# Kernel tuning notes

Hardware: AMD Instinct MI355X
Metric: run time of the kernel (lower is better)

Reference implementation:

```python
import jax, jax.numpy as jnp
import numpy as np

BSZ, KDIM, UDIM, T = 2048, 64, 16, 30


def setup_inputs() -> dict:
    key = jax.random.key(0)
    k0, k1, k2, k3, k4 = jax.random.split(key, 5)
    I_k = jnp.eye(KDIM, dtype=jnp.float32)
    I_u = jnp.eye(UDIM, dtype=jnp.float32)
    # Stabilized dynamics (spectral radius ~<1) so the T-step Riccati recursion stays finite.
    A = 0.9 * I_k + 0.02 * jax.random.normal(k0, (BSZ, KDIM, KDIM), dtype=jnp.float32)
    B = 0.1 * jax.random.normal(k1, (BSZ, KDIM, UDIM), dtype=jnp.float32)
    q = 0.1 * jax.random.normal(k2, (BSZ, KDIM, KDIM), dtype=jnp.float32)
    Q = jnp.einsum('bij,bkj->bik', q, q) + I_k  # SPD cost
    r = 0.1 * jax.random.normal(k3, (BSZ, UDIM, UDIM), dtype=jnp.float32)
    R = jnp.einsum('bij,bkj->bik', r, r) + I_u  # SPD control cost
    goals = jax.random.normal(k4, (BSZ, T + 1, KDIM), dtype=jnp.float32)
    return {"A": A, "B": B, "Q": Q, "R": R, "goals": goals}


def reference(A, B, Q, R, goals):
    # Faithful port of KoopmanLQR._solve_lqr: backward Riccati recursion.
    T_h = goals.shape[1] - 1
    AT = jnp.swapaxes(A, -2, -1)
    BT = jnp.swapaxes(B, -2, -1)
    V0 = Q
    v0 = jnp.einsum('bij,bj->bi', Q, goals[:, -1, :])
    # time-major goals for steps T-1 .. 0 (reversed)
    goals_rev = jnp.swapaxes(goals[:, :T_h, :], 0, 1)[::-1]  # [T, B, k]

    def step(carry, goal_i):
        V, v = carry
        Vuu = BT @ V @ B + R                         # [B,u,u]
        Vuu_inv = jnp.linalg.pinv(Vuu)
        Kg = Vuu_inv @ BT @ V @ A                    # [B,u,k] feedback gain
        kg = jnp.einsum('bij,bj->bi', Vuu_inv @ BT, v)  # [B,u] feedforward
        A_BK = A - B @ Kg
        V_new = AT @ V @ A_BK + Q
        v_new = jnp.einsum('bji,bj->bi', A_BK, v) + jnp.einsum('bij,bj->bi', Q, goal_i)
        return (V_new, v_new), (Kg, kg)

    (_, _), (K_rev, k_rev) = jax.lax.scan(step, (V0, v0), goals_rev)
    K_all = K_rev[::-1]  # [T,B,u,k], K_all[i] == K[i] of the torch loop
    k_all = k_rev[::-1]  # [T,B,u]
    # pack gains and feedforward terms in one array: [T,B,u,k+1]
    return jnp.concatenate([K_all, k_all[..., None]], axis=-1)
```

## Files before the change

### kernel.cpp

```cpp
#include <hip/hip_runtime.h>

#define KD 64
#define UD 16
#define TH 30
#define NT 256

typedef short bf16x8 __attribute__((ext_vector_type(8)));
typedef float f32x4 __attribute__((ext_vector_type(4)));
typedef unsigned short u16x4 __attribute__((ext_vector_type(4)));

__device__ __forceinline__ void f2hl(float f, unsigned short& h, unsigned short& l) {
  unsigned int ub = __float_as_uint(f);
  h = (unsigned short)(ub >> 16);
  float fh = __uint_as_float(ub & 0xffff0000u);
  l = (unsigned short)(__float_as_uint(f - fh) >> 16);
}
__device__ __forceinline__ float rec(unsigned short h, unsigned short l) {
  return __uint_as_float((unsigned int)h << 16) + __uint_as_float((unsigned int)l << 16);
}

__device__ __forceinline__ bf16x8 ld64(const unsigned short* buf, int row, int kcg) {
  return *(const bf16x8*)(buf + row * 64 + ((kcg ^ (row & 7)) << 3));
}
__device__ __forceinline__ bf16x8 ld16(const unsigned short* buf, int row, int g) {
  if (g < 2) return *(const bf16x8*)(buf + row * 16 + (g << 3));
  bf16x8 z = {};
  return z;
}
__device__ __forceinline__ void st64_4(unsigned short* buf, int row, int col0, u16x4 v) {
  int off = row * 64 + ((((col0 >> 3)) ^ (row & 7)) << 3) + (col0 & 7);
  *(u16x4*)(buf + off) = v;
}
__device__ __forceinline__ void st16_4(unsigned short* buf, int row, int col0, u16x4 v) {
  *(u16x4*)(buf + row * 16 + col0) = v;
}
__device__ __forceinline__ void cvt4(f32x4 a, u16x4& h, u16x4& l) {
  #pragma unroll
  for (int i = 0; i < 4; ++i) {
    unsigned short hh, ll;
    f2hl(a[i], hh, ll);
    h[i] = hh; l[i] = ll;
  }
}

#define MFMA3(ACC, XH, XL, YH, YL)                                          \
  ACC = __builtin_amdgcn_mfma_f32_16x16x32_bf16(XH, YH, ACC, 0, 0, 0);      \
  ACC = __builtin_amdgcn_mfma_f32_16x16x32_bf16(XH, YL, ACC, 0, 0, 0);      \
  ACC = __builtin_amdgcn_mfma_f32_16x16x32_bf16(XL, YH, ACC, 0, 0, 0);

__global__ __launch_bounds__(NT, 2) void lqr_mfma(
    const float* __restrict__ gA, const float* __restrict__ gB,
    const float* __restrict__ gQ, const float* __restrict__ gR,
    const float* __restrict__ gG, float* __restrict__ gOut, int bsz)
{
  __shared__ unsigned short sVh[64 * 64], sVl[64 * 64];
  __shared__ unsigned short sAth[64 * 64], sAtl[64 * 64];
  __shared__ unsigned short sWth[64 * 64], sWtl[64 * 64];
  __shared__ unsigned short sBth[16 * 64], sBtl[16 * 64];
  __shared__ unsigned short sVBh[16 * 64], sVBl[16 * 64];
  __shared__ unsigned short sBWh[64 * 16], sBWl[64 * 16];
  __shared__ unsigned short sKth[64 * 16], sKtl[64 * 16];
  __shared__ unsigned short sVIh[16 * 16], sVIl[16 * 16];
  __shared__ float sQG[(TH + 1) * 64];
  __shared__ float sVuu[16 * 17];
  __shared__ float sMT[16 * 17];
  __shared__ float sKg[16 * 65];
  __shared__ float sv[64];
  __shared__ float sBtv[16];

  const int b    = blockIdx.x;
  const int tid  = threadIdx.x;
  const int lane = tid & 63;
  const int wv   = tid >> 6;
  const int r    = lane & 15;
  const int g    = lane >> 4;

  const float* Ab = gA + (size_t)b * (64 * 64);
  const float* Bb = gB + (size_t)b * (64 * 16);
  const float* Qb = gQ + (size_t)b * (64 * 64);
  const float* Rb = gR + (size_t)b * (16 * 16);
  const float* Gb = gG + (size_t)b * ((TH + 1) * 64);

  for (int idx = tid; idx < 64 * 64; idx += NT) {
    int k = idx >> 6, i = idx & 63;
    unsigned short h, l;
    f2hl(Ab[idx], h, l);
    int offA = i * 64 + ((((k >> 3)) ^ (i & 7)) << 3) + (k & 7);
    sAth[offA] = h; sAtl[offA] = l;
    f2hl(Qb[idx], h, l);
    int offV = k * 64 + ((((i >> 3)) ^ (k & 7)) << 3) + (i & 7);
    sVh[offV] = h; sVl[offV] = l;
  }
  for (int idx = tid; idx < 64 * 16; idx += NT) {
    int k = idx >> 4, u = idx & 15;
    unsigned short h, l;
    f2hl(Bb[idx], h, l);
    int off = u * 64 + ((((k >> 3)) ^ (u & 7)) << 3) + (k & 7);
    sBth[off] = h; sBtl[off] = l;
  }
  __syncthreads();

  for (int idx = tid; idx < (TH + 1) * 64; idx += NT) {
    int t = idx >> 6, i = idx & 63;
    const float* gt = Gb + t * 64;
    float s = 0.f;
    #pragma unroll 8
    for (int k = 0; k < 64; ++k) {
      int off = i * 64 + ((((k >> 3)) ^ (i & 7)) << 3) + (k & 7);
      s += rec(sVh[off], sVl[off]) * gt[k];
    }
    sQG[idx] = s;
  }
  __syncthreads();
  if (tid < 64) sv[tid] = sQG[TH * 64 + tid];

  f32x4 qreg[4];
  #pragma unroll
  for (int c = 0; c < 4; ++c) {
    #pragma unroll
    for (int rg = 0; rg < 4; ++rg)
      qreg[c][rg] = Qb[(16 * wv + 4 * g + rg) * 64 + 16 * c + r];
  }
  f32x4 rreg;
  #pragma unroll
  for (int rg = 0; rg < 4; ++rg) rreg[rg] = Rb[(4 * g + rg) * 16 + r];

  for (int t = TH - 1; t >= 0; --t) {
    {
      f32x4 accW0 = 0.f, accW1 = 0.f, accW2 = 0.f, accW3 = 0.f, accVB = 0.f;
      #pragma unroll
      for (int kc = 0; kc < 2; ++kc) {
        int kcg = 4 * kc + g;
        bf16x8 xh = ld64(sVh, 16 * wv + r, kcg);
        bf16x8 xl = ld64(sVl, 16 * wv + r, kcg);
        bf16x8 yh, yl;
        yh = ld64(sAth, 0 * 16 + r, kcg); yl = ld64(sAtl, 0 * 16 + r, kcg);
        MFMA3(accW0, xh, xl, yh, yl)
        yh = ld64(sAth, 1 * 16 + r, kcg); yl = ld64(sAtl, 1 * 16 + r, kcg);
        MFMA3(accW1, xh, xl, yh, yl)
        yh = ld64(sAth, 2 * 16 + r, kcg); yl = ld64(sAtl, 2 * 16 + r, kcg);
        MFMA3(accW2, xh, xl, yh, yl)
        yh = ld64(sAth, 3 * 16 + r, kcg); yl = ld64(sAtl, 3 * 16 + r, kcg);
        MFMA3(accW3, xh, xl, yh, yl)
        yh = ld64(sBth, r, kcg); yl = ld64(sBtl, r, kcg);
        MFMA3(accVB, xh, xl, yh, yl)
      }
      u16x4 h4, l4;
      cvt4(accW0, h4, l4); st64_4(sWth, 0 * 16 + r, 16 * wv + 4 * g, h4); st64_4(sWtl, 0 * 16 + r, 16 * wv + 4 * g, l4);
      cvt4(accW1, h4, l4); st64_4(sWth, 1 * 16 + r, 16 * wv + 4 * g, h4); st64_4(sWtl, 1 * 16 + r, 16 * wv + 4 * g, l4);
      cvt4(accW2, h4, l4); st64_4(sWth, 2 * 16 + r, 16 * wv + 4 * g, h4); st64_4(sWtl, 2 * 16 + r, 16 * wv + 4 * g, l4);
      cvt4(accW3, h4, l4); st64_4(sWth, 3 * 16 + r, 16 * wv + 4 * g, h4); st64_4(sWtl, 3 * 16 + r, 16 * wv + 4 * g, l4);
      cvt4(accVB, h4, l4); st64_4(sVBh, r, 16 * wv + 4 * g, h4); st64_4(sVBl, r, 16 * wv + 4 * g, l4);
    }
    __syncthreads();

    if (wv == 0) {
      f32x4 accU = rreg, accBv = 0.f;
      #pragma unroll
      for (int kc = 0; kc < 2; ++kc) {
        int kcg = 4 * kc + g;
        bf16x8 xh = ld64(sBth, r, kcg);
        bf16x8 xl = ld64(sBtl, r, kcg);
        bf16x8 yh = ld64(sVBh, r, kcg);
        bf16x8 yl = ld64(sVBl, r, kcg);
        MFMA3(accU, xh, xl, yh, yl)
        bf16x8 vh = {}, vl = {};
        if (r == 0) {
          #pragma unroll
          for (int e = 0; e < 8; ++e) {
            unsigned short hh, ll;
            f2hl(sv[32 * kc + 8 * g + e], hh, ll);
            vh[e] = (short)hh; vl[e] = (short)ll;
          }
        }
        MFMA3(accBv, xh, xl, vh, vl)
      }
      #pragma unroll
      for (int rg = 0; rg < 4; ++rg) sVuu[(4 * g + rg) * 17 + r] = accU[rg];
      if (r == 0) {
        #pragma unroll
        for (int rg = 0; rg < 4; ++rg) sBtv[4 * g + rg] = accBv[rg];
      }
    } else {
      #pragma unroll
      for (int ci = 0; ci < 2; ++ci) {
        int c = (ci == 0) ? (wv - 1) : ((wv == 1) ? 3 : -1);
        if (c >= 0) {
          f32x4 acc = 0.f;
          #pragma unroll
          for (int kc = 0; kc < 2; ++kc) {
            int kcg = 4 * kc + g;
            bf16x8 xh = ld64(sBth, r, kcg);
            bf16x8 xl = ld64(sBtl, r, kcg);
            bf16x8 yh = ld64(sWth, 16 * c + r, kcg);
            bf16x8 yl = ld64(sWtl, 16 * c + r, kcg);
            MFMA3(acc, xh, xl, yh, yl)
          }
          u16x4 h4, l4; cvt4(acc, h4, l4);
          st16_4(sBWh, 16 * c + r, 4 * g, h4);
          st16_4(sBWl, 16 * c + r, 4 * g, l4);
        }
      }
    }
    __syncthreads();

    if (wv == 0) {
      const int u = lane & 15;
      float rr[16];
      #pragma unroll
      for (int k = 0; k < 16; ++k) rr[k] = sVuu[u * 17 + k];
      #pragma unroll
      for (int j = 0; j < 16; ++j) {
        float s = rr[j];
        #pragma unroll
        for (int k = 0; k < j; ++k) s -= rr[k] * __shfl(rr[k], j);
        const float dj  = sqrtf(__shfl(s, j));
        const float inv = 1.f / dj;
        rr[j] = (u == j) ? dj : s * inv;
      }
      float idia[16];
      #pragma unroll
      for (int i = 0; i < 16; ++i) idia[i] = 1.f / __shfl(rr[i], i);
      float x[16];
      #pragma unroll
      for (int i = 0; i < 16; ++i) {
        float s = (i == u) ? 1.f : 0.f;
        #pragma unroll
        for (int k = 0; k < i; ++k) s -= __shfl(rr[k], i) * x[k];
        x[i] = s * idia[i];
      }
      if (lane < 16) {
        #pragma unroll
        for (int i = 0; i < 16; ++i) sMT[u * 17 + i] = x[i];
      }
    }
    __syncthreads();

    {
      const int a2 = tid & 15, b2 = tid >> 4;
      float s = 0.f;
      #pragma unroll
      for (int i = 0; i < 16; ++i) s += sMT[a2 * 17 + i] * sMT[b2 * 17 + i];
      unsigned short h, l; f2hl(s, h, l);
      sVIh[a2 * 16 + b2] = h; sVIl[a2 * 16 + b2] = l;
    }
    __syncthreads();

    {
      f32x4 acc = 0.f;
      bf16x8 xh = ld16(sVIh, r, g);
      bf16x8 xl = ld16(sVIl, r, g);
      bf16x8 yh = ld16(sBWh, 16 * wv + r, g);
      bf16x8 yl = ld16(sBWl, 16 * wv + r, g);
      MFMA3(acc, xh, xl, yh, yl)
      u16x4 h4, l4;
      f32x4 nacc = -acc;
      cvt4(nacc, h4, l4);
      st16_4(sKth, 16 * wv + r, 4 * g, h4);
      st16_4(sKtl, 16 * wv + r, 4 * g, l4);
      #pragma unroll
      for (int rg = 0; rg < 4; ++rg)
        sKg[(4 * g + rg) * 65 + (16 * wv + r)] = acc[rg];
      if (tid >= 64 && tid < 80) {
        const int uu = tid - 64;
        float s = 0.f;
        #pragma unroll
        for (int w2 = 0; w2 < 16; ++w2)
          s += rec(sVIh[uu * 16 + w2], sVIl[uu * 16 + w2]) * sBtv[w2];
        sKg[uu * 65 + 64] = s;
      }
    }
    __syncthreads();

    {
      const size_t obase = ((size_t)t * bsz + b) * (16 * 65);
      for (int idx = tid; idx < 16 * 65; idx += NT)
        gOut[obase + idx] = sKg[idx];
    }
    if (t > 0) {
      f32x4 acc0 = qreg[0], acc1 = qreg[1], acc2 = qreg[2], acc3 = qreg[3];
      {
        bf16x8 x2h = ld16(sBWh, 16 * wv + r, g);
        bf16x8 x2l = ld16(sBWl, 16 * wv + r, g);
        bf16x8 yh, yl;
        yh = ld16(sKth, 0 * 16 + r, g); yl = ld16(sKtl, 0 * 16 + r, g);
        MFMA3(acc0, x2h, x2l, yh, yl)
        yh = ld16(sKth, 1 * 16 + r, g); yl = ld16(sKtl, 1 * 16 + r, g);
        MFMA3(acc1, x2h, x2l, yh, yl)
        yh = ld16(sKth, 2 * 16 + r, g); yl = ld16(sKtl, 2 * 16 + r, g);
        MFMA3(acc2, x2h, x2l, yh, yl)
        yh = ld16(sKth, 3 * 16 + r, g); yl = ld16(sKtl, 3 * 16 + r, g);
        MFMA3(acc3, x2h, x2l, yh, yl)
      }
      #pragma unroll
      for (int kc = 0; kc < 2; ++kc) {
        int kcg = 4 * kc + g;
        bf16x8 xh = ld64(sAth, 16 * wv + r, kcg);
        bf16x8 xl = ld64(sAtl, 16 * wv + r, kcg);
        bf16x8 yh, yl;
        yh = ld64(sWth, 0 * 16 + r, kcg); yl = ld64(sWtl, 0 * 16 + r, kcg);
        MFMA3(acc0, xh, xl, yh, yl)
        yh = ld64(sWth, 1 * 16 + r, kcg); yl = ld64(sWtl, 1 * 16 + r, kcg);
        MFMA3(acc1, xh, xl, yh, yl)
        yh = ld64(sWth, 2 * 16 + r, kcg); yl = ld64(sWtl, 2 * 16 + r, kcg);
        MFMA3(acc2, xh, xl, yh, yl)
        yh = ld64(sWth, 3 * 16 + r, kcg); yl = ld64(sWtl, 3 * 16 + r, kcg);
        MFMA3(acc3, xh, xl, yh, yl)
      }
      {
        const int i = tid & 63, q = tid >> 6;
        float s = (q == 0) ? sQG[t * 64 + i] : 0.f;
        #pragma unroll
        for (int kk = 0; kk < 16; ++kk) {
          int k = 16 * q + kk;
          int off = i * 64 + ((((k >> 3)) ^ (i & 7)) << 3) + (k & 7);
          s += rec(sAth[off], sAtl[off]) * sv[k];
        }
        #pragma unroll
        for (int uu = 0; uu < 4; ++uu)
          s -= sKg[(4 * q + uu) * 65 + i] * sBtv[4 * q + uu];
        sMT[q * 64 + i] = s;
      }
      u16x4 h4, l4;
      cvt4(acc0, h4, l4); st64_4(sVh, 0 * 16 + r, 16 * wv + 4 * g, h4); st64_4(sVl, 0 * 16 + r, 16 * wv + 4 * g, l4);
      cvt4(acc1, h4, l4); st64_4(sVh, 1 * 16 + r, 16 * wv + 4 * g, h4); st64_4(sVl, 1 * 16 + r, 16 * wv + 4 * g, l4);
      cvt4(acc2, h4, l4); st64_4(sVh, 2 * 16 + r, 16 * wv + 4 * g, h4); st64_4(sVl, 2 * 16 + r, 16 * wv + 4 * g, l4);
      cvt4(acc3, h4, l4); st64_4(sVh, 3 * 16 + r, 16 * wv + 4 * g, h4); st64_4(sVl, 3 * 16 + r, 16 * wv + 4 * g, l4);
      __syncthreads();
      if (tid < 64)
        sv[tid] = sMT[tid] + sMT[64 + tid] + sMT[128 + tid] + sMT[192 + tid];
    }
  }
}

extern "C" void kernel_launch(void* const* d_in, const int* in_sizes, int n_in,
                              void* d_out, int out_size, void* d_ws, size_t ws_size,
                              hipStream_t stream) {
  (void)n_in; (void)out_size; (void)d_ws; (void)ws_size;
  const float* A = (const float*)d_in[0];
  const float* B = (const float*)d_in[1];
  const float* Q = (const float*)d_in[2];
  const float* R = (const float*)d_in[3];
  const float* G = (const float*)d_in[4];
  float* out = (float*)d_out;
  const int bsz = in_sizes[3] / (UD * UD);
  lqr_mfma<<<bsz, NT, 0, stream>>>(A, B, Q, R, G, out, bsz);
}
```

Before: 961.4 us.

## Double block to eight waves and overlap Riccati sub-steps across waves

Moves the kernel from 256 to 512 threads per block and re-partitions each Riccati step so different waves run independent sub-computations at the same time. The A^T·W product overlaps with the Vuu inversion and the B^T·W products, A^T·v moves to MFMA on idle waves, and Q·goals is precomputed with MFMA. The v update is rewritten using B·W and Kg·v instead of a dot with sKg, and gains go straight to global memory without staging through shared memory. BW and K tiles are padded to row stride 24, presumably to reduce bank conflicts. The cost is more waves per block and extra barriers, and the launch bound now targets 4 blocks per CU.

```diff
diff --git a/kernel.cpp b/kernel.cpp
--- a/kernel.cpp
+++ b/kernel.cpp
@@ -1,9 +1,7 @@
 #include <hip/hip_runtime.h>
 
-#define KD 64
-#define UD 16
 #define TH 30
-#define NT 256
+#define NT 512
 
 typedef short bf16x8 __attribute__((ext_vector_type(8)));
 typedef float f32x4 __attribute__((ext_vector_type(4)));
@@ -18,21 +16,24 @@
 __device__ __forceinline__ float rec(unsigned short h, unsigned short l) {
   return __uint_as_float((unsigned int)h << 16) + __uint_as_float((unsigned int)l << 16);
 }
-
 __device__ __forceinline__ bf16x8 ld64(const unsigned short* buf, int row, int kcg) {
   return *(const bf16x8*)(buf + row * 64 + ((kcg ^ (row & 7)) << 3));
 }
-__device__ __forceinline__ bf16x8 ld16(const unsigned short* buf, int row, int g) {
+__device__ __forceinline__ void st64_4(unsigned short* buf, int row, int col0, u16x4 v) {
+  *(u16x4*)(buf + row * 64 + (((col0 >> 3) ^ (row & 7)) << 3) + (col0 & 7)) = v;
+}
+__device__ __forceinline__ bf16x8 ld24(const unsigned short* buf, int row, int g) {
+  if (g < 2) return *(const bf16x8*)(buf + row * 24 + (g << 3));
+  bf16x8 z = {};
+  return z;
+}
+__device__ __forceinline__ void st24_4(unsigned short* buf, int row, int col0, u16x4 v) {
+  *(u16x4*)(buf + row * 24 + col0) = v;
+}
+__device__ __forceinline__ bf16x8 ld16v(const unsigned short* buf, int row, int g) {
   if (g < 2) return *(const bf16x8*)(buf + row * 16 + (g << 3));
   bf16x8 z = {};
   return z;
-}
-__device__ __forceinline__ void st64_4(unsigned short* buf, int row, int col0, u16x4 v) {
-  int off = row * 64 + ((((col0 >> 3)) ^ (row & 7)) << 3) + (col0 & 7);
-  *(u16x4*)(buf + off) = v;
-}
-__device__ __forceinline__ void st16_4(unsigned short* buf, int row, int col0, u16x4 v) {
-  *(u16x4*)(buf + row * 16 + col0) = v;
 }
 __device__ __forceinline__ void cvt4(f32x4 a, u16x4& h, u16x4& l) {
   #pragma unroll
@@ -43,28 +44,29 @@
   }
 }
 
-#define MFMA3(ACC, XH, XL, YH, YL)                                          \
-  ACC = __builtin_amdgcn_mfma_f32_16x16x32_bf16(XH, YH, ACC, 0, 0, 0);      \
-  ACC = __builtin_amdgcn_mfma_f32_16x16x32_bf16(XH, YL, ACC, 0, 0, 0);      \
+#define MFMA3(ACC, XH, XL, YH, YL)                                        \
+  ACC = __builtin_amdgcn_mfma_f32_16x16x32_bf16(XH, YH, ACC, 0, 0, 0);    \
+  ACC = __builtin_amdgcn_mfma_f32_16x16x32_bf16(XH, YL, ACC, 0, 0, 0);    \
   ACC = __builtin_amdgcn_mfma_f32_16x16x32_bf16(XL, YH, ACC, 0, 0, 0);
 
-__global__ __launch_bounds__(NT, 2) void lqr_mfma(
+__global__ __launch_bounds__(NT, 4) void lqr8(
     const float* __restrict__ gA, const float* __restrict__ gB,
     const float* __restrict__ gQ, const float* __restrict__ gR,
     const float* __restrict__ gG, float* __restrict__ gOut, int bsz)
 {
-  __shared__ unsigned short sVh[64 * 64], sVl[64 * 64];
-  __shared__ unsigned short sAth[64 * 64], sAtl[64 * 64];
-  __shared__ unsigned short sWth[64 * 64], sWtl[64 * 64];
-  __shared__ unsigned short sBth[16 * 64], sBtl[16 * 64];
-  __shared__ unsigned short sVBh[16 * 64], sVBl[16 * 64];
-  __shared__ unsigned short sBWh[64 * 16], sBWl[64 * 16];
-  __shared__ unsigned short sKth[64 * 16], sKtl[64 * 16];
-  __shared__ unsigned short sVIh[16 * 16], sVIl[16 * 16];
-  __shared__ float sQG[(TH + 1) * 64];
+  __shared__ unsigned short sVh[4096], sVl[4096];
+  __shared__ unsigned short sAth[4096], sAtl[4096];
+  __shared__ unsigned short sWth[4096], sWtl[4096];
+  __shared__ unsigned short sBth[1024], sBtl[1024];
+  __shared__ unsigned short sVBh[1024], sVBl[1024];
+  __shared__ unsigned short sBWh[64 * 24], sBWl[64 * 24];
+  __shared__ unsigned short sKth[64 * 24], sKtl[64 * 24];
+  __shared__ unsigned short sVIh[256], sVIl[256];
+  __shared__ float sQG[31 * 64];
   __shared__ float sVuu[16 * 17];
   __shared__ float sMT[16 * 17];
-  __shared__ float sKg[16 * 65];
+  __shared__ float sVp[64];
+  __shared__ float sKgv[16];
   __shared__ float sv[64];
   __shared__ float sBtv[16];
 
@@ -74,88 +76,120 @@
   const int wv   = tid >> 6;
   const int r    = lane & 15;
   const int g    = lane >> 4;
-
-  const float* Ab = gA + (size_t)b * (64 * 64);
-  const float* Bb = gB + (size_t)b * (64 * 16);
-  const float* Qb = gQ + (size_t)b * (64 * 64);
-  const float* Rb = gR + (size_t)b * (16 * 16);
+  const int it   = wv & 3;
+  const int h    = wv >> 2;
+  const int c0   = 2 * h, c1 = 2 * h + 1;
+
+  const float* Ab = gA + (size_t)b * 4096;
+  const float* Bb = gB + (size_t)b * 1024;
+  const float* Qb = gQ + (size_t)b * 4096;
+  const float* Rb = gR + (size_t)b * 256;
   const float* Gb = gG + (size_t)b * ((TH + 1) * 64);
 
-  for (int idx = tid; idx < 64 * 64; idx += NT) {
+  for (int idx = tid; idx < 4096; idx += NT) {
     int k = idx >> 6, i = idx & 63;
-    unsigned short h, l;
-    f2hl(Ab[idx], h, l);
-    int offA = i * 64 + ((((k >> 3)) ^ (i & 7)) << 3) + (k & 7);
-    sAth[offA] = h; sAtl[offA] = l;
-    f2hl(Qb[idx], h, l);
-    int offV = k * 64 + ((((i >> 3)) ^ (k & 7)) << 3) + (i & 7);
-    sVh[offV] = h; sVl[offV] = l;
-  }
-  for (int idx = tid; idx < 64 * 16; idx += NT) {
+    unsigned short hh, ll;
+    f2hl(Ab[idx], hh, ll);
+    int offA = i * 64 + (((k >> 3) ^ (i & 7)) << 3) + (k & 7);
+    sAth[offA] = hh; sAtl[offA] = ll;
+    f2hl(Qb[idx], hh, ll);
+    int offV = k * 64 + (((i >> 3) ^ (k & 7)) << 3) + (i & 7);
+    sVh[offV] = hh; sVl[offV] = ll;
+  }
+  for (int idx = tid; idx < 1024; idx += NT) {
     int k = idx >> 4, u = idx & 15;
-    unsigned short h, l;
-    f2hl(Bb[idx], h, l);
-    int off = u * 64 + ((((k >> 3)) ^ (u & 7)) << 3) + (k & 7);
-    sBth[off] = h; sBtl[off] = l;
+    unsigned short hh, ll;
+    f2hl(Bb[idx], hh, ll);
+    int off = u * 64 + (((k >> 3) ^ (u & 7)) << 3) + (k & 7);
+    sBth[off] = hh; sBtl[off] = ll;
+  }
+  for (int idx = tid; idx < 2048; idx += NT) {
+    int t = idx >> 6, k = idx & 63;
+    float val = (t <= TH) ? Gb[idx] : 0.f;
+    unsigned short hh, ll;
+    f2hl(val, hh, ll);
+    int off = t * 64 + (((k >> 3) ^ (t & 7)) << 3) + (k & 7);
+    sWth[off] = hh; sWtl[off] = ll;
   }
   __syncthreads();
 
-  for (int idx = tid; idx < (TH + 1) * 64; idx += NT) {
-    int t = idx >> 6, i = idx & 63;
-    const float* gt = Gb + t * 64;
-    float s = 0.f;
-    #pragma unroll 8
-    for (int k = 0; k < 64; ++k) {
-      int off = i * 64 + ((((k >> 3)) ^ (i & 7)) << 3) + (k & 7);
-      s += rec(sVh[off], sVl[off]) * gt[k];
-    }
-    sQG[idx] = s;
+  {
+    f32x4 acc = {};
+    #pragma unroll
+    for (int kc = 0; kc < 2; ++kc) {
+      int kcg = 4 * kc + g;
+      bf16x8 xh = ld64(sWth, 16 * h + r, kcg);
+      bf16x8 xl = ld64(sWtl, 16 * h + r, kcg);
+      bf16x8 yh = ld64(sVh, 16 * it + r, kcg);
+      bf16x8 yl = ld64(sVl, 16 * it + r, kcg);
+      MFMA3(acc, xh, xl, yh, yl)
+    }
+    #pragma unroll
+    for (int rg = 0; rg < 4; ++rg) {
+      int tt = 16 * h + 4 * g + rg;
+      if (tt <= TH) sQG[tt * 64 + 16 * it + r] = acc[rg];
+    }
   }
   __syncthreads();
   if (tid < 64) sv[tid] = sQG[TH * 64 + tid];
 
-  f32x4 qreg[4];
+  f32x4 qreg0, qreg1, rreg;
   #pragma unroll
-  for (int c = 0; c < 4; ++c) {
-    #pragma unroll
-    for (int rg = 0; rg < 4; ++rg)
-      qreg[c][rg] = Qb[(16 * wv + 4 * g + rg) * 64 + 16 * c + r];
-  }
-  f32x4 rreg;
-  #pragma unroll
-  for (int rg = 0; rg < 4; ++rg) rreg[rg] = Rb[(4 * g + rg) * 16 + r];
-
+  for (int rg = 0; rg < 4; ++rg) {
+    qreg0[rg] = Qb[(16 * it + 4 * g + rg) * 64 + 16 * c0 + r];
+    qreg1[rg] = Qb[(16 * it + 4 * g + rg) * 64 + 16 * c1 + r];
+    rreg[rg]  = Rb[(4 * g + rg) * 16 + r];
+  }
+
+  #pragma unroll 1
   for (int t = TH - 1; t >= 0; --t) {
+    f32x4 vacc0 = qreg0, vacc1 = qreg1;
+
+    auto ATW = [&]() {
+      #pragma unroll
+      for (int kc = 0; kc < 2; ++kc) {
+        int kcg = 4 * kc + g;
+        bf16x8 xh = ld64(sAth, 16 * it + r, kcg);
+        bf16x8 xl = ld64(sAtl, 16 * it + r, kcg);
+        bf16x8 yh = ld64(sWth, 16 * c0 + r, kcg);
+        bf16x8 yl = ld64(sWtl, 16 * c0 + r, kcg);
+        MFMA3(vacc0, xh, xl, yh, yl)
+        yh = ld64(sWth, 16 * c1 + r, kcg);
+        yl = ld64(sWtl, 16 * c1 + r, kcg);
+        MFMA3(vacc1, xh, xl, yh, yl)
+      }
+    };
+
     {
-      f32x4 accW0 = 0.f, accW1 = 0.f, accW2 = 0.f, accW3 = 0.f, accVB = 0.f;
-      #pragma unroll
-      for (int kc = 0; kc < 2; ++kc) {
-        int kcg = 4 * kc + g;
-        bf16x8 xh = ld64(sVh, 16 * wv + r, kcg);
-        bf16x8 xl = ld64(sVl, 16 * wv + r, kcg);
-        bf16x8 yh, yl;
-        yh = ld64(sAth, 0 * 16 + r, kcg); yl = ld64(sAtl, 0 * 16 + r, kcg);
-        MFMA3(accW0, xh, xl, yh, yl)
-        yh = ld64(sAth, 1 * 16 + r, kcg); yl = ld64(sAtl, 1 * 16 + r, kcg);
-        MFMA3(accW1, xh, xl, yh, yl)
-        yh = ld64(sAth, 2 * 16 + r, kcg); yl = ld64(sAtl, 2 * 16 + r, kcg);
-        MFMA3(accW2, xh, xl, yh, yl)
-        yh = ld64(sAth, 3 * 16 + r, kcg); yl = ld64(sAtl, 3 * 16 + r, kcg);
-        MFMA3(accW3, xh, xl, yh, yl)
-        yh = ld64(sBth, r, kcg); yl = ld64(sBtl, r, kcg);
-        MFMA3(accVB, xh, xl, yh, yl)
+      f32x4 aW0 = {}, aW1 = {}, aVB = {};
+      #pragma unroll
+      for (int kc = 0; kc < 2; ++kc) {
+        int kcg = 4 * kc + g;
+        bf16x8 xh = ld64(sVh, 16 * it + r, kcg);
+        bf16x8 xl = ld64(sVl, 16 * it + r, kcg);
+        bf16x8 yh = ld64(sAth, 16 * c0 + r, kcg);
+        bf16x8 yl = ld64(sAtl, 16 * c0 + r, kcg);
+        MFMA3(aW0, xh, xl, yh, yl)
+        yh = ld64(sAth, 16 * c1 + r, kcg);
+        yl = ld64(sAtl, 16 * c1 + r, kcg);
+        MFMA3(aW1, xh, xl, yh, yl)
+        if (h == 0) {
+          yh = ld64(sBth, r, kcg);
+          yl = ld64(sBtl, r, kcg);
+          MFMA3(aVB, xh, xl, yh, yl)
+        }
       }
       u16x4 h4, l4;
-      cvt4(accW0, h4, l4); st64_4(sWth, 0 * 16 + r, 16 * wv + 4 * g, h4); st64_4(sWtl, 0 * 16 + r, 16 * wv + 4 * g, l4);
-      cvt4(accW1, h4, l4); st64_4(sWth, 1 * 16 + r, 16 * wv + 4 * g, h4); st64_4(sWtl, 1 * 16 + r, 16 * wv + 4 * g, l4);
-      cvt4(accW2, h4, l4); st64_4(sWth, 2 * 16 + r, 16 * wv + 4 * g, h4); st64_4(sWtl, 2 * 16 + r, 16 * wv + 4 * g, l4);
-      cvt4(accW3, h4, l4); st64_4(sWth, 3 * 16 + r, 16 * wv + 4 * g, h4); st64_4(sWtl, 3 * 16 + r, 16 * wv + 4 * g, l4);
-      cvt4(accVB, h4, l4); st64_4(sVBh, r, 16 * wv + 4 * g, h4); st64_4(sVBl, r, 16 * wv + 4 * g, l4);
+      cvt4(aW0, h4, l4); st64_4(sWth, 16 * c0 + r, 16 * it + 4 * g, h4); st64_4(sWtl, 16 * c0 + r, 16 * it + 4 * g, l4);
+      cvt4(aW1, h4, l4); st64_4(sWth, 16 * c1 + r, 16 * it + 4 * g, h4); st64_4(sWtl, 16 * c1 + r, 16 * it + 4 * g, l4);
+      if (h == 0) {
+        cvt4(aVB, h4, l4); st64_4(sVBh, r, 16 * it + 4 * g, h4); st64_4(sVBl, r, 16 * it + 4 * g, l4);
+      }
     }
     __syncthreads();
 
     if (wv == 0) {
-      f32x4 accU = rreg, accBv = 0.f;
+      f32x4 accU = rreg;
       #pragma unroll
       for (int kc = 0; kc < 2; ++kc) {
         int kcg = 4 * kc + g;
@@ -164,6 +198,16 @@
         bf16x8 yh = ld64(sVBh, r, kcg);
         bf16x8 yl = ld64(sVBl, r, kcg);
         MFMA3(accU, xh, xl, yh, yl)
+      }
+      #pragma unroll
+      for (int rg = 0; rg < 4; ++rg) sVuu[(4 * g + rg) * 17 + r] = accU[rg];
+    } else if (wv == 1) {
+      f32x4 accBv = {};
+      #pragma unroll
+      for (int kc = 0; kc < 2; ++kc) {
+        int kcg = 4 * kc + g;
+        bf16x8 xh = ld64(sBth, r, kcg);
+        bf16x8 xl = ld64(sBtl, r, kcg);
         bf16x8 vh = {}, vl = {};
         if (r == 0) {
           #pragma unroll
@@ -175,37 +219,32 @@
         }
         MFMA3(accBv, xh, xl, vh, vl)
       }
-      #pragma unroll
-      for (int rg = 0; rg < 4; ++rg) sVuu[(4 * g + rg) * 17 + r] = accU[rg];
       if (r == 0) {
         #pragma unroll
         for (int rg = 0; rg < 4; ++rg) sBtv[4 * g + rg] = accBv[rg];
       }
-    } else {
-      #pragma unroll
-      for (int ci = 0; ci < 2; ++ci) {
-        int c = (ci == 0) ? (wv - 1) : ((wv == 1) ? 3 : -1);
-        if (c >= 0) {
-          f32x4 acc = 0.f;
-          #pragma unroll
-          for (int kc = 0; kc < 2; ++kc) {
-            int kcg = 4 * kc + g;
-            bf16x8 xh = ld64(sBth, r, kcg);
-            bf16x8 xl = ld64(sBtl, r, kcg);
-            bf16x8 yh = ld64(sWth, 16 * c + r, kcg);
-            bf16x8 yl = ld64(sWtl, 16 * c + r, kcg);
-            MFMA3(acc, xh, xl, yh, yl)
-          }
-          u16x4 h4, l4; cvt4(acc, h4, l4);
-          st16_4(sBWh, 16 * c + r, 4 * g, h4);
-          st16_4(sBWl, 16 * c + r, 4 * g, l4);
-        }
-      }
+    } else if (wv <= 5) {
+      const int c = wv - 2;
+      f32x4 acc = {};
+      #pragma unroll
+      for (int kc = 0; kc < 2; ++kc) {
+        int kcg = 4 * kc + g;
+        bf16x8 xh = ld64(sBth, r, kcg);
+        bf16x8 xl = ld64(sBtl, r, kcg);
+        bf16x8 yh = ld64(sWth, 16 * c + r, kcg);
+        bf16x8 yl = ld64(sWtl, 16 * c + r, kcg);
+        MFMA3(acc, xh, xl, yh, yl)
+      }
+      u16x4 h4, l4; cvt4(acc, h4, l4);
+      st24_4(sBWh, 16 * c + r, 4 * g, h4);
+      st24_4(sBWl, 16 * c + r, 4 * g, l4);
+    } else if (t > 0) {
+      ATW();
     }
     __syncthreads();
 
     if (wv == 0) {
-      const int u = lane & 15;
+      const int u = r;
       float rr[16];
       #pragma unroll
       for (int k = 0; k < 16; ++k) rr[k] = sVuu[u * 17 + k];
@@ -233,103 +272,108 @@
         #pragma unroll
         for (int i = 0; i < 16; ++i) sMT[u * 17 + i] = x[i];
       }
-    }
-    __syncthreads();
-
-    {
-      const int a2 = tid & 15, b2 = tid >> 4;
+    } else if (wv <= 5) {
+      if (t > 0) ATW();
+    } else if (t > 0) {
+      const int rt0 = 2 * (wv - 6), rt1 = rt0 + 1;
+      f32x4 at0 = {}, at1 = {};
+      #pragma unroll
+      for (int kc = 0; kc < 2; ++kc) {
+        int kcg = 4 * kc + g;
+        bf16x8 vh = {}, vl = {};
+        if (r == 0) {
+          #pragma unroll
+          for (int e = 0; e < 8; ++e) {
+            unsigned short hh, ll;
+            f2hl(sv[32 * kc + 8 * g + e], hh, ll);
+            vh[e] = (short)hh; vl[e] = (short)ll;
+          }
+        }
+        bf16x8 xh = ld64(sAth, 16 * rt0 + r, kcg);
+        bf16x8 xl = ld64(sAtl, 16 * rt0 + r, kcg);
+        MFMA3(at0, xh, xl, vh, vl)
+        xh = ld64(sAth, 16 * rt1 + r, kcg);
+        xl = ld64(sAtl, 16 * rt1 + r, kcg);
+        MFMA3(at1, xh, xl, vh, vl)
+      }
+      if (r == 0) {
+        #pragma unroll
+        for (int rg = 0; rg < 4; ++rg) {
+          sVp[16 * rt0 + 4 * g + rg] = at0[rg];
+          sVp[16 * rt1 + 4 * g + rg] = at1[rg];
+        }
+      }
+    }
+    __syncthreads();
+
+    if (wv == 1 || wv == 2) {
+      const int e = (wv - 1) * 64 + lane;
+      const int a2 = e & 15, b2 = e >> 4;
+      float s0 = 0.f, s1 = 0.f;
+      #pragma unroll
+      for (int i = 0; i < 16; ++i) {
+        const float ma = sMT[a2 * 17 + i];
+        s0 += ma * sMT[b2 * 17 + i];
+        s1 += ma * sMT[(b2 + 8) * 17 + i];
+      }
+      unsigned short hh, ll;
+      f2hl(s0, hh, ll); sVIh[a2 * 16 + b2] = hh;     sVIl[a2 * 16 + b2] = ll;
+      f2hl(s1, hh, ll); sVIh[a2 * 16 + b2 + 8] = hh; sVIl[a2 * 16 + b2 + 8] = ll;
+    } else if (wv == 0 && t > 0) {
+      ATW();
+    }
+    __syncthreads();
+
+    const size_t obase = ((size_t)t * bsz + b) * (16 * 65);
+    if (wv < 4) {
+      const int c = wv;
+      f32x4 acc = {};
+      bf16x8 xh = ld16v(sVIh, r, g);
+      bf16x8 xl = ld16v(sVIl, r, g);
+      bf16x8 yh = ld24(sBWh, 16 * c + r, g);
+      bf16x8 yl = ld24(sBWl, 16 * c + r, g);
+      MFMA3(acc, xh, xl, yh, yl)
+      f32x4 nacc = -acc;
+      u16x4 h4, l4; cvt4(nacc, h4, l4);
+      st24_4(sKth, 16 * c + r, 4 * g, h4);
+      st24_4(sKtl, 16 * c + r, 4 * g, l4);
+      #pragma unroll
+      for (int rg = 0; rg < 4; ++rg)
+        gOut[obase + (size_t)(4 * g + rg) * 65 + 16 * c + r] = acc[rg];
+    } else if (wv == 4 && lane < 16) {
       float s = 0.f;
       #pragma unroll
-      for (int i = 0; i < 16; ++i) s += sMT[a2 * 17 + i] * sMT[b2 * 17 + i];
-      unsigned short h, l; f2hl(s, h, l);
-      sVIh[a2 * 16 + b2] = h; sVIl[a2 * 16 + b2] = l;
-    }
-    __syncthreads();
-
-    {
-      f32x4 acc = 0.f;
-      bf16x8 xh = ld16(sVIh, r, g);
-      bf16x8 xl = ld16(sVIl, r, g);
-      bf16x8 yh = ld16(sBWh, 16 * wv + r, g);
-      bf16x8 yl = ld16(sBWl, 16 * wv + r, g);
-      MFMA3(acc, xh, xl, yh, yl)
+      for (int w2 = 0; w2 < 16; ++w2)
+        s += rec(sVIh[lane * 16 + w2], sVIl[lane * 16 + w2]) * sBtv[w2];
+      sKgv[lane] = s;
+      gOut[obase + (size_t)lane * 65 + 64] = s;
+    }
+    __syncthreads();
+
+    if (t > 0) {
+      {
+        bf16x8 x2h = ld24(sBWh, 16 * it + r, g);
+        bf16x8 x2l = ld24(sBWl, 16 * it + r, g);
+        bf16x8 yh = ld24(sKth, 16 * c0 + r, g);
+        bf16x8 yl = ld24(sKtl, 16 * c0 + r, g);
+        MFMA3(vacc0, x2h, x2l, yh, yl)
+        yh = ld24(sKth, 16 * c1 + r, g);
+        yl = ld24(sKtl, 16 * c1 + r, g);
+        MFMA3(vacc1, x2h, x2l, yh, yl)
+      }
       u16x4 h4, l4;
-      f32x4 nacc = -acc;
-      cvt4(nacc, h4, l4);
-      st16_4(sKth, 16 * wv + r, 4 * g, h4);
-      st16_4(sKtl, 16 * wv + r, 4 * g, l4);
-      #pragma unroll
-      for (int rg = 0; rg < 4; ++rg)
-        sKg[(4 * g + rg) * 65 + (16 * wv + r)] = acc[rg];
-      if (tid >= 64 && tid < 80) {
-        const int uu = tid - 64;
-        float s = 0.f;
-        #pragma unroll
-        for (int w2 = 0; w2 < 16; ++w2)
-          s += rec(sVIh[uu * 16 + w2], sVIl[uu * 16 + w2]) * sBtv[w2];
-        sKg[uu * 65 + 64] = s;
-      }
-    }
-    __syncthreads();
-
-    {
-      const size_t obase = ((size_t)t * bsz + b) * (16 * 65);
-      for (int idx = tid; idx < 16 * 65; idx += NT)
-        gOut[obase + idx] = sKg[idx];
-    }
-    if (t > 0) {
-      f32x4 acc0 = qreg[0], acc1 = qreg[1], acc2 = qreg[2], acc3 = qreg[3];
-      {
-        bf16x8 x2h = ld16(sBWh, 16 * wv + r, g);
-        bf16x8 x2l = ld16(sBWl, 16 * wv + r, g);
-        bf16x8 yh, yl;
-        yh = ld16(sKth, 0 * 16 + r, g); yl = ld16(sKtl, 0 * 16 + r, g);
-        MFMA3(acc0, x2h, x2l, yh, yl)
-        yh = ld16(sKth, 1 * 16 + r, g); yl = ld16(sKtl, 1 * 16 + r, g);
-        MFMA3(acc1, x2h, x2l, yh, yl)
-        yh = ld16(sKth, 2 * 16 + r, g); yl = ld16(sKtl, 2 * 16 + r, g);
-        MFMA3(acc2, x2h, x2l, yh, yl)
-        yh = ld16(sKth, 3 * 16 + r, g); yl = ld16(sKtl, 3 * 16 + r, g);
-        MFMA3(acc3, x2h, x2l, yh, yl)
-      }
-      #pragma unroll
-      for (int kc = 0; kc < 2; ++kc) {
-        int kcg = 4 * kc + g;
-        bf16x8 xh = ld64(sAth, 16 * wv + r, kcg);
-        bf16x8 xl = ld64(sAtl, 16 * wv + r, kcg);
-        bf16x8 yh, yl;
-        yh = ld64(sWth, 0 * 16 + r, kcg); yl = ld64(sWtl, 0 * 16 + r, kcg);
-        MFMA3(acc0, xh, xl, yh, yl)
-        yh = ld64(sWth, 1 * 16 + r, kcg); yl = ld64(sWtl, 1 * 16 + r, kcg);
-        MFMA3(acc1, xh, xl, yh, yl)
-        yh = ld64(sWth, 2 * 16 + r, kcg); yl = ld64(sWtl, 2 * 16 + r, kcg);
-        MFMA3(acc2, xh, xl, yh, yl)
-        yh = ld64(sWth, 3 * 16 + r, kcg); yl = ld64(sWtl, 3 * 16 + r, kcg);
-        MFMA3(acc3, xh, xl, yh, yl)
-      }
-      {
-        const int i = tid & 63, q = tid >> 6;
-        float s = (q == 0) ? sQG[t * 64 + i] : 0.f;
-        #pragma unroll
-        for (int kk = 0; kk < 16; ++kk) {
-          int k = 16 * q + kk;
-          int off = i * 64 + ((((k >> 3)) ^ (i & 7)) << 3) + (k & 7);
-          s += rec(sAth[off], sAtl[off]) * sv[k];
-        }
-        #pragma unroll
-        for (int uu = 0; uu < 4; ++uu)
-          s -= sKg[(4 * q + uu) * 65 + i] * sBtv[4 * q + uu];
-        sMT[q * 64 + i] = s;
-      }
-      u16x4 h4, l4;
-      cvt4(acc0, h4, l4); st64_4(sVh, 0 * 16 + r, 16 * wv + 4 * g, h4); st64_4(sVl, 0 * 16 + r, 16 * wv + 4 * g, l4);
-      cvt4(acc1, h4, l4); st64_4(sVh, 1 * 16 + r, 16 * wv + 4 * g, h4); st64_4(sVl, 1 * 16 + r, 16 * wv + 4 * g, l4);
-      cvt4(acc2, h4, l4); st64_4(sVh, 2 * 16 + r, 16 * wv + 4 * g, h4); st64_4(sVl, 2 * 16 + r, 16 * wv + 4 * g, l4);
-      cvt4(acc3, h4, l4); st64_4(sVh, 3 * 16 + r, 16 * wv + 4 * g, h4); st64_4(sVl, 3 * 16 + r, 16 * wv + 4 * g, l4);
-      __syncthreads();
-      if (tid < 64)
-        sv[tid] = sMT[tid] + sMT[64 + tid] + sMT[128 + tid] + sMT[192 + tid];
-    }
+      cvt4(vacc0, h4, l4); st64_4(sVh, 16 * c0 + r, 16 * it + 4 * g, h4); st64_4(sVl, 16 * c0 + r, 16 * it + 4 * g, l4);
+      cvt4(vacc1, h4, l4); st64_4(sVh, 16 * c1 + r, 16 * it + 4 * g, h4); st64_4(sVl, 16 * c1 + r, 16 * it + 4 * g, l4);
+      if (wv == 5) {
+        const int i = lane;
+        float s = sQG[t * 64 + i] + sVp[i];
+        #pragma unroll
+        for (int u2 = 0; u2 < 16; ++u2)
+          s -= rec(sBWh[i * 24 + u2], sBWl[i * 24 + u2]) * sKgv[u2];
+        sv[i] = s;
+      }
+    }
+    __syncthreads();
   }
 }
 
@@ -343,6 +387,6 @@
   const float* R = (const float*)d_in[3];
   const float* G = (const float*)d_in[4];
   float* out = (float*)d_out;
-  const int bsz = in_sizes[3] / (UD * UD);
-  lqr_mfma<<<bsz, NT, 0, stream>>>(A, B, Q, R, G, out, bsz);
-}
+  const int bsz = in_sizes[3] / 256;
+  lqr8<<<bsz, NT, 0, stream>>>(A, B, Q, R, G, out, bsz);
+}
```

Result: slower. 2.060 ms (+114.3%).
